# Kernel optimization log

Hardware: AMD Instinct MI355X
Metric: run time of the kernel (lower is better)

Reference implementation:

```python
import jax, jax.numpy as jnp
import numpy as np

STRIDE, K, PAD = 2, 4, 1
DN = ('NCH', 'OIH', 'NCH')


def conv1d(x, w, b):
    # w: (out, in, k); stride-2, pad-1 conv matching nn.Conv1d(k=4,s=2,p=1)
    y = jax.lax.conv_general_dilated(x, w, (STRIDE,), ((PAD, PAD),), dimension_numbers=DN)
    return y + b[None, :, None]


def conv_transpose1d(x, w, b):
    # w: (in, out, k) torch ConvTranspose1d layout. Equivalent forward conv:
    # dilate input by stride, pad k-1-p=2 each side, flipped+transposed kernel.
    wf = jnp.flip(w, -1).transpose(1, 0, 2)  # (out, in, k)
    y = jax.lax.conv_general_dilated(x, wf, (1,), ((K - 1 - PAD, K - 1 - PAD),),
                                     lhs_dilation=(STRIDE,), dimension_numbers=DN)
    return y + b[None, :, None]


def setup_inputs() -> dict:
    key = jax.random.key(0)
    ks = jax.random.split(key, 9)
    s = 0.1  # keep activations stable through 6 layers
    return {
        'x': jax.random.normal(ks[0], (16, 1, 65536), dtype=jnp.float32),
        'enc_w0': jax.random.normal(ks[1], (64, 1, 4), dtype=jnp.float32) * s,
        'enc_w': jax.random.normal(ks[2], (5, 64, 64, 4), dtype=jnp.float32) * s,
        'enc_b': jax.random.normal(ks[3], (6, 64), dtype=jnp.float32) * s,
        'codebook': jax.random.normal(ks[4], (1024, 64), dtype=jnp.float32),
        'dec_w': jax.random.normal(ks[5], (5, 64, 64, 4), dtype=jnp.float32) * s,
        'dec_w_last': jax.random.normal(ks[6], (64, 1, 4), dtype=jnp.float32) * s,
        'dec_b': jax.random.normal(ks[7], (5, 64), dtype=jnp.float32) * s,
        'dec_b_last': jax.random.normal(ks[8], (1,), dtype=jnp.float32) * s,
    }


def reference(x, enc_w0, enc_w, enc_b, codebook, dec_w, dec_w_last, dec_b, dec_b_last):
    B = x.shape[0]
    D = codebook.shape[1]

    h = jax.nn.relu(conv1d(x, enc_w0, enc_b[0]))
    for i in range(5):
        h = jax.nn.relu(conv1d(h, enc_w[i], enc_b[i + 1]))
    # h: (B, D, L'); flatten tokens
    z_e = h.transpose(0, 2, 1).reshape(-1, D)  # (B*L', D)

    # ---- Vector quantize: squared-distance argmin + gather ----
    dist = (jnp.sum(z_e * z_e, axis=1, keepdims=True)
            - 2.0 * z_e @ codebook.T
            + jnp.sum(codebook * codebook, axis=1)[None, :])  # (B*L', C)
    ids = jnp.argmin(dist, axis=-1)
    e = codebook[ids]
    e_k = z_e + jax.lax.stop_gradient(e - z_e)  # straight-through

    g = e_k.reshape(B, -1, D).transpose(0, 2, 1)  # (B, D, L')

    for i in range(5):
        g = jax.nn.relu(conv_transpose1d(g, dec_w[i], dec_b[i]))
    y = conv_transpose1d(g, dec_w_last, dec_b_last)
    return y, z_e, ids
```

## Files before the change

### kernel.cpp

```cpp
#include <hip/hip_runtime.h>

#define CH 64
#define TILE 128

typedef short s16x8 __attribute__((ext_vector_type(8)));
typedef float f32x4 __attribute__((ext_vector_type(4)));

static __device__ __forceinline__ ushort f2bf(float f) {
    union { float f; uint u; } v; v.f = f;
    const uint r = (v.u + 0x7FFFu + ((v.u >> 16) & 1u)) >> 16;
    return (ushort)r;
}
static __device__ __forceinline__ float bf2f(ushort u) {
    union { uint u; float f; } v; v.u = ((uint)u) << 16; return v.f;
}

__global__ __launch_bounds__(256) void k_prepack_enc(
    const float* __restrict__ enc_w, float* __restrict__ encW)
{
    const int idx = blockIdx.x * 256 + threadIdx.x;
    const int tau = idx & 3;
    const int o = (idx >> 2) & 63;
    const int i = (idx >> 8) & 63;
    const int L = idx >> 14;
    encW[idx] = enc_w[(((size_t)L * 64 + o) * 64 + i) * 4 + tau];
}

__device__ __forceinline__ void stage_half(
    const float* __restrict__ inb, float (*inT)[264], int half,
    int m0, int Lin, int tid)
{
    const int r = tid >> 3;
    const int i = half * 32 + r;
    const int seg = tid & 7;
    const float* src = inb + (size_t)i * Lin + 2 * m0 + 32 * seg;
    float* dst = inT[r] + 1 + 32 * seg;
#pragma unroll
    for (int t = 0; t < 8; ++t) {
        const float4 v = *(const float4*)(src + 4 * t);
        float* d = dst + 4 * t;
        d[0] = v.x;
        *(float2*)(d + 1) = make_float2(v.y, v.z);
        d[3] = v.w;
    }
    if (tid < 64) {
        const int rr = tid & 31, side = tid >> 5;
        const int pl = side ? 257 : 0;
        const int p = 2 * m0 - 1 + pl;
        inT[rr][pl] = (p >= 0 && p < Lin) ? inb[(size_t)(half * 32 + rr) * Lin + p] : 0.f;
    }
}

__device__ __forceinline__ void conv_accum_half(
    const float (*inT)[264], const float* __restrict__ wpk, int ibase,
    float acc[4][8], int og, int pg)
{
    const float* wI = wpk + og * 16 + (size_t)ibase * 256;
    for (int ii = 0; ii < 32; ++ii) {
        const float* wp = wI + ii * 256;
        const float4 w0 = *(const float4*)(wp + 0);
        const float4 w1 = *(const float4*)(wp + 4);
        const float4 w2 = *(const float4*)(wp + 8);
        const float4 w3 = *(const float4*)(wp + 12);
        const float* row = inT[ii];
#pragma unroll
        for (int j = 0; j < 4; ++j) {
            const int base = 4 * pg + 64 * j;
            const float2 xa = *(const float2*)(row + base);
            const float2 xb = *(const float2*)(row + base + 2);
            const float2 xc = *(const float2*)(row + base + 4);
            acc[0][2*j]   += w0.x * xa.x + w0.y * xa.y + w0.z * xb.x + w0.w * xb.y;
            acc[1][2*j]   += w1.x * xa.x + w1.y * xa.y + w1.z * xb.x + w1.w * xb.y;
            acc[2][2*j]   += w2.x * xa.x + w2.y * xa.y + w2.z * xb.x + w2.w * xb.y;
            acc[3][2*j]   += w3.x * xa.x + w3.y * xa.y + w3.z * xb.x + w3.w * xb.y;
            acc[0][2*j+1] += w0.x * xb.x + w0.y * xb.y + w0.z * xc.x + w0.w * xc.y;
            acc[1][2*j+1] += w1.x * xb.x + w1.y * xb.y + w1.z * xc.x + w1.w * xc.y;
            acc[2][2*j+1] += w2.x * xb.x + w2.y * xb.y + w2.z * xc.x + w2.w * xc.y;
            acc[3][2*j+1] += w3.x * xb.x + w3.y * xb.y + w3.z * xc.x + w3.w * xc.y;
        }
    }
}

__device__ __forceinline__ void conv_epilogue(
    float acc[4][8], float* __restrict__ out,
    int b, int m0, int Lout, int transpose, int og, int pg)
{
    if (!transpose) {
#pragma unroll
        for (int oo = 0; oo < 4; ++oo) {
            float* ob = out + ((size_t)b * CH + og * 4 + oo) * Lout + m0 + 2 * pg;
#pragma unroll
            for (int j = 0; j < 4; ++j) {
                float2 v;
                v.x = fmaxf(acc[oo][2*j], 0.f);
                v.y = fmaxf(acc[oo][2*j+1], 0.f);
                *(float2*)(ob + 32 * j) = v;
            }
        }
    } else {
#pragma unroll
        for (int j = 0; j < 4; ++j)
#pragma unroll
            for (int h = 0; h < 2; ++h) {
                const int ml = 2 * pg + 32 * j + h;
                float* ob = out + ((size_t)b * Lout + m0 + ml) * CH + og * 4;
                float4 v;
                v.x = fmaxf(acc[0][2*j+h], 0.f);
                v.y = fmaxf(acc[1][2*j+h], 0.f);
                v.z = fmaxf(acc[2][2*j+h], 0.f);
                v.w = fmaxf(acc[3][2*j+h], 0.f);
                *(float4*)ob = v;
            }
    }
}

__global__ __launch_bounds__(256) void k_enc_conv(
    const float* __restrict__ in, const float* __restrict__ wpk,
    const float* __restrict__ bias, float* __restrict__ out,
    int Lin, int Lout, int transpose)
{
    __shared__ float inT[32][264];
    const int m0 = blockIdx.x * TILE;
    const int b = blockIdx.y;
    const int tid = threadIdx.x;
    const int og = tid >> 4, pg = tid & 15;
    const float* inb = in + (size_t)b * CH * Lin;
    float acc[4][8];
#pragma unroll
    for (int oo = 0; oo < 4; ++oo) {
        const float bv = bias[og * 4 + oo];
#pragma unroll
        for (int j = 0; j < 8; ++j) acc[oo][j] = bv;
    }
    stage_half(inb, inT, 0, m0, Lin, tid);
    __syncthreads();
    conv_accum_half(inT, wpk, 0, acc, og, pg);
    __syncthreads();
    stage_half(inb, inT, 1, m0, Lin, tid);
    __syncthreads();
    conv_accum_half(inT, wpk, 32, acc, og, pg);
    conv_epilogue(acc, out, b, m0, Lout, transpose, og, pg);
}

__global__ __launch_bounds__(256) void k_enc01(
    const float* __restrict__ x, const float* __restrict__ w0,
    const float* __restrict__ b0, const float* __restrict__ wpk0,
    const float* __restrict__ b1, float* __restrict__ out)
{
    __shared__ float xl[520];
    __shared__ float e0s[32][264];
    const int m0 = blockIdx.x * TILE;
    const int b = blockIdx.y;
    const int tid = threadIdx.x;
    const int og = tid >> 4, pg = tid & 15;
    const float* xb = x + (size_t)b * 65536;
    const int x0i = 4 * m0 - 3;
    for (int xi = tid; xi < 518; xi += 256) {
        const int q = x0i + xi;
        xl[xi] = (q >= 0 && q < 65536) ? xb[q] : 0.f;
    }
    float acc[4][8];
#pragma unroll
    for (int oo = 0; oo < 4; ++oo) {
        const float bv = b1[og * 4 + oo];
#pragma unroll
        for (int j = 0; j < 8; ++j) acc[oo][j] = bv;
    }
    const int r = tid >> 3;
    const int oct = tid & 7;
    const int pbase = 2 * m0 - 1;
    __syncthreads();
    for (int half = 0; half < 2; ++half) {
        {
            const int i = half * 32 + r;
            const float4 wv = *(const float4*)(w0 + i * 4);
            const float bv = b0[i];
            for (int t = 0; t < 33; ++t) {
                const int pl = oct * 33 + t;
                if (pl < 258) {
                    const int pe = pbase + pl;
                    const float* xp = xl + 2 * pl;
                    const float v = wv.x * xp[0] + wv.y * xp[1] + wv.z * xp[2] + wv.w * xp[3] + bv;
                    e0s[r][pl] = (pe >= 0 && pe < 32768) ? fmaxf(v, 0.f) : 0.f;
                }
            }
        }
        __syncthreads();
        conv_accum_half(e0s, wpk0, half * 32, acc, og, pg);
        __syncthreads();
    }
    conv_epilogue(acc, out, b, m0, 16384, 0, og, pg);
}

__global__ __launch_bounds__(512) void k_vq(
    const float* __restrict__ z, const float* __restrict__ cb,
    float* __restrict__ idsf, float* __restrict__ g)
{
    __shared__ float c2s[1024];
    __shared__ float rval[8][64];
    __shared__ int   ridx[8][64];
    __shared__ int   widx[64];
    const int t0 = blockIdx.x * 64;
    const int tid = threadIdx.x;
    const int lane = tid & 63;
    const int wv = __builtin_amdgcn_readfirstlane(tid >> 6);

    for (int c = tid; c < 1024; c += 512) {
        const float* cp = cb + (size_t)c * 64;
        float s0 = 0.f, s1 = 0.f, s2 = 0.f, s3 = 0.f;
#pragma unroll
        for (int d = 0; d < 64; d += 4) {
            const float4 v = *(const float4*)(cp + d);
            s0 += v.x * v.x; s1 += v.y * v.y; s2 += v.z * v.z; s3 += v.w * v.w;
        }
        c2s[c] = (s0 + s1) + (s2 + s3);
    }
    float pz[64];
    {
        const float* zp = z + (size_t)(t0 + lane) * 64;
#pragma unroll
        for (int d = 0; d < 64; d += 4) {
            const float4 v = *(const float4*)(zp + d);
            pz[d] = -2.f * v.x; pz[d + 1] = -2.f * v.y;
            pz[d + 2] = -2.f * v.z; pz[d + 3] = -2.f * v.w;
        }
    }
    __syncthreads();
    float best = 3.0e38f; int bidx = 0;
    const int cbase = wv * 128;
    for (int cc = 0; cc < 128; ++cc) {
        const int code = cbase + cc;
        const float* cp = cb + (size_t)code * 64;
        float a0 = 0.f, a1 = 0.f, a2 = 0.f, a3 = 0.f;
#pragma unroll
        for (int d = 0; d < 64; d += 4) {
            a0 += cp[d] * pz[d];
            a1 += cp[d + 1] * pz[d + 1];
            a2 += cp[d + 2] * pz[d + 2];
            a3 += cp[d + 3] * pz[d + 3];
        }
        const float dist = c2s[code] + ((a0 + a1) + (a2 + a3));
        if (dist < best) { best = dist; bidx = code; }
    }
    rval[wv][lane] = best; ridx[wv][lane] = bidx;
    __syncthreads();
    if (tid < 64) {
        float bv = rval[0][tid]; int bi = ridx[0][tid];
#pragma unroll
        for (int k2 = 1; k2 < 8; ++k2) {
            const float v = rval[k2][tid];
            if (v < bv) { bv = v; bi = ridx[k2][tid]; }
        }
        widx[tid] = bi;
        idsf[t0 + tid] = (float)bi;
    }
    __syncthreads();
    const int bb = t0 >> 10;
    const int mb = t0 & 1023;
    for (int e = tid; e < 4096; e += 512) {
        const int tok = e & 63;
        const int d = e >> 6;
        g[((size_t)bb * CH + d) * 1024 + mb + tok] = cb[(size_t)widx[tok] * 64 + d];
    }
}

__global__ __launch_bounds__(256) void k_prepack(
    const float* __restrict__ dec_w, ushort* __restrict__ Afrag)
{
    const int idx = blockIdx.x * 256 + threadIdx.x;
    const int j    = idx & 7;
    const int lane = (idx >> 3) & 63;
    const int kt   = (idx >> 9) & 1;
    const int m    = (idx >> 10) & 3;
    const int tap  = (idx >> 12) & 3;
    const int L    = idx >> 14;
    const int o = m * 16 + (lane & 15);
    const int i = kt * 32 + ((lane >> 4) << 3) + j;
    Afrag[idx] = f2bf(dec_w[(((size_t)L * 64 + i) * 64 + o) * 4 + tap]);
}

__device__ __forceinline__ void stage_X(
    const float* __restrict__ Xb, ushort* __restrict__ Xs, int u0, int Lin, int tid)
{
    for (int e = tid; e < 272; e += 256) {
        const int i4 = (e & 15) * 4;
        const int u4 = e >> 4;
        const int bu = u0 - 2 + 4 * u4;
        float v[4][4];
        if (bu >= 0 && bu + 3 < Lin) {
            const float* src = Xb + (size_t)i4 * Lin + bu;
#pragma unroll
            for (int di = 0; di < 4; ++di) {
                const float4 t = *(const float4*)(src + (size_t)di * Lin);
                v[di][0] = t.x; v[di][1] = t.y; v[di][2] = t.z; v[di][3] = t.w;
            }
        } else {
#pragma unroll
            for (int di = 0; di < 4; ++di)
#pragma unroll
                for (int du = 0; du < 4; ++du) {
                    const int u = bu + du;
                    v[di][du] = (u >= 0 && u < Lin) ? Xb[(size_t)(i4 + di) * Lin + u] : 0.f;
                }
        }
#pragma unroll
        for (int du = 0; du < 4; ++du) {
            ushort4 pk;
            pk.x = f2bf(v[0][du]); pk.y = f2bf(v[1][du]);
            pk.z = f2bf(v[2][du]); pk.w = f2bf(v[3][du]);
            *(ushort4*)(Xs + (size_t)(4 * u4 + du) * 72 + i4) = pk;
        }
    }
}

__device__ __forceinline__ void dec_mfma_compute(
    const ushort* __restrict__ Xs, const ushort* __restrict__ AfragL,
    int tid, f32x4 accE[4], f32x4 accO[4], int& ul_out, int& kg_out, int& lane_out)
{
    const int lane = tid & 63;
    const int wave = tid >> 6;
    const int col = lane & 15, kg = lane >> 4;
    const int ul = wave * 16 + col;
    const ushort* basep = Xs + kg * 8;
    s16x8 Bm1[2], B0[2], Bp1[2];
#pragma unroll
    for (int kt = 0; kt < 2; ++kt) {
        Bm1[kt] = *(const s16x8*)(basep + (ul + 1) * 72 + kt * 32);
        B0[kt]  = *(const s16x8*)(basep + (ul + 2) * 72 + kt * 32);
        Bp1[kt] = *(const s16x8*)(basep + (ul + 3) * 72 + kt * 32);
    }
    const s16x8* Af = (const s16x8*)AfragL;
#pragma unroll
    for (int m = 0; m < 4; ++m) {
        f32x4 aE = {0.f, 0.f, 0.f, 0.f};
        f32x4 aO = {0.f, 0.f, 0.f, 0.f};
#pragma unroll
        for (int kt = 0; kt < 2; ++kt) {
            aE = __builtin_amdgcn_mfma_f32_16x16x32_bf16(
                Af[((1 * 4 + m) * 2 + kt) * 64 + lane], B0[kt], aE, 0, 0, 0);
            aE = __builtin_amdgcn_mfma_f32_16x16x32_bf16(
                Af[((3 * 4 + m) * 2 + kt) * 64 + lane], Bm1[kt], aE, 0, 0, 0);
            aO = __builtin_amdgcn_mfma_f32_16x16x32_bf16(
                Af[((2 * 4 + m) * 2 + kt) * 64 + lane], B0[kt], aO, 0, 0, 0);
            aO = __builtin_amdgcn_mfma_f32_16x16x32_bf16(
                Af[((0 * 4 + m) * 2 + kt) * 64 + lane], Bp1[kt], aO, 0, 0, 0);
        }
        accE[m] = aE;
        accO[m] = aO;
    }
    ul_out = ul; kg_out = kg; lane_out = lane;
}

__global__ __launch_bounds__(256) void k_dec2(
    const float* __restrict__ X, const ushort* __restrict__ AfragL,
    const float* __restrict__ bias, float* __restrict__ Y, int Lin)
{
    __shared__ ushort Xs[68 * 72];
    const int u0 = blockIdx.x * 64;
    const int b  = blockIdx.y;
    const int tid = threadIdx.x;
    const int Lout = Lin * 2;
    stage_X(X + (size_t)b * CH * Lin, Xs, u0, Lin, tid);
    __syncthreads();
    f32x4 accE[4], accO[4];
    int ul, kg, lane;
    dec_mfma_compute(Xs, AfragL, tid, accE, accO, ul, kg, lane);
    const int n2 = 2 * (u0 + ul);
#pragma unroll
    for (int m = 0; m < 4; ++m) {
        const float4 bm4 = *(const float4*)(bias + m * 16 + kg * 4);
        const float bb[4] = {bm4.x, bm4.y, bm4.z, bm4.w};
        float* yo = Y + ((size_t)b * CH + m * 16 + kg * 4) * Lout + n2;
#pragma unroll
        for (int r = 0; r < 4; ++r) {
            float2 v;
            v.x = fmaxf(accE[m][r] + bb[r], 0.f);
            v.y = fmaxf(accO[m][r] + bb[r], 0.f);
            *(float2*)(yo + (size_t)r * Lout) = v;
        }
    }
}

__global__ __launch_bounds__(256) void k_dec4y(
    const float* __restrict__ X, const ushort* __restrict__ AfragL,
    const float* __restrict__ w4, const float* __restrict__ bias,
    const float* __restrict__ wl, const float* __restrict__ blp,
    float* __restrict__ y)
{
    __shared__ ushort Xs[68 * 72];
    __shared__ float d4s[64][130];
    const int u0 = blockIdx.x * 64;
    const int b  = blockIdx.y;
    const int tid = threadIdx.x;
    const int Lin = 16384;
    stage_X(X + (size_t)b * CH * Lin, Xs, u0, Lin, tid);
    __syncthreads();
    f32x4 accE[4], accO[4];
    int ul, kg, lane;
    dec_mfma_compute(Xs, AfragL, tid, accE, accO, ul, kg, lane);
#pragma unroll
    for (int m = 0; m < 4; ++m) {
        const float4 bm4 = *(const float4*)(bias + m * 16 + kg * 4);
        const float bb[4] = {bm4.x, bm4.y, bm4.z, bm4.w};
#pragma unroll
        for (int r = 0; r < 4; ++r) {
            const int o = m * 16 + kg * 4 + r;
            d4s[o][2 * ul + 1] = fmaxf(accE[m][r] + bb[r], 0.f);
            d4s[o][2 * ul + 2] = fmaxf(accO[m][r] + bb[r], 0.f);
        }
    }
    {
        const int side = tid >> 7;
        const int o = (tid >> 1) & 63;
        const int half = tid & 1;
        const int ib = half * 32;
        float part = 0.f;
        if (side == 0) {
            for (int i = ib; i < ib + 32; ++i) {
                const float xu = bf2f(Xs[1 * 72 + i]);
                const float xp = bf2f(Xs[2 * 72 + i]);
                const float* wp = w4 + ((size_t)i * 64 + o) * 4;
                part += wp[2] * xu + wp[0] * xp;
            }
        } else {
            for (int i = ib; i < ib + 32; ++i) {
                const float xu = bf2f(Xs[66 * 72 + i]);
                const float xm = bf2f(Xs[65 * 72 + i]);
                const float* wp = w4 + ((size_t)i * 64 + o) * 4;
                part += wp[1] * xu + wp[3] * xm;
            }
        }
        part += __shfl_xor(part, 1);
        if (half == 0) {
            const float acc = bias[o] + part;
            if (side == 0) d4s[o][0]   = (u0 > 0)          ? fmaxf(acc, 0.f) : 0.f;
            else           d4s[o][129] = (u0 + 64 < 16384) ? fmaxf(acc, 0.f) : 0.f;
        }
    }
    __syncthreads();
    {
        const int odd = tid & 1;
        const int vl = (tid >> 1) + 1;
        float acc = blp[0];
        for (int o = 0; o < 64; ++o) {
            const float4 wv = *(const float4*)(wl + o * 4);
            const float xv = d4s[o][vl];
            const float xn = d4s[o][odd ? vl + 1 : vl - 1];
            acc += odd ? (wv.z * xv + wv.x * xn) : (wv.y * xv + wv.w * xn);
        }
        y[(size_t)b * 65536 + 4 * u0 + tid] = acc;
    }
}

extern "C" void kernel_launch(void* const* d_in, const int* in_sizes, int n_in,
                              void* d_out, int out_size, void* d_ws, size_t ws_size,
                              hipStream_t stream) {
    const float* x      = (const float*)d_in[0];
    const float* enc_w0 = (const float*)d_in[1];
    const float* enc_w  = (const float*)d_in[2];
    const float* enc_b  = (const float*)d_in[3];
    const float* cb     = (const float*)d_in[4];
    const float* dec_w  = (const float*)d_in[5];
    const float* dec_wl = (const float*)d_in[6];
    const float* dec_b  = (const float*)d_in[7];
    const float* dec_bl = (const float*)d_in[8];
    float* y    = (float*)d_out;
    float* z_e  = y + 1048576;
    float* idsf = y + 2097152;

    float* A  = (float*)d_ws;
    float* Bf = A + 16777216;

    float*  encW  = y + 14 * 65536;
    ushort* Afrag = (ushort*)(encW + 81920);

    k_prepack_enc<<<dim3(320), 256, 0, stream>>>(enc_w, encW);
    k_prepack<<<dim3(320), 256, 0, stream>>>(dec_w, Afrag);

    k_enc01<<<dim3(128, 16), 256, 0, stream>>>(x, enc_w0, enc_b, encW, enc_b + 64, A);
    k_enc_conv<<<dim3(64, 16), 256, 0, stream>>>(A,  encW + 1 * 16384, enc_b + 2 * 64, Bf, 16384, 8192, 0);
    k_enc_conv<<<dim3(32, 16), 256, 0, stream>>>(Bf, encW + 2 * 16384, enc_b + 3 * 64, A,  8192,  4096, 0);
    k_enc_conv<<<dim3(16, 16), 256, 0, stream>>>(A,  encW + 3 * 16384, enc_b + 4 * 64, Bf, 4096,  2048, 0);
    k_enc_conv<<<dim3(8, 16),  256, 0, stream>>>(Bf, encW + 4 * 16384, enc_b + 5 * 64, z_e, 2048, 1024, 1);
    k_vq<<<256, 512, 0, stream>>>(z_e, cb, idsf, A);

    k_dec2<<<dim3(16, 16),  256, 0, stream>>>(A,  Afrag + 0 * 16384, dec_b + 0 * 64, Bf, 1024);
    k_dec2<<<dim3(32, 16),  256, 0, stream>>>(Bf, Afrag + 1 * 16384, dec_b + 1 * 64, A,  2048);
    k_dec2<<<dim3(64, 16),  256, 0, stream>>>(A,  Afrag + 2 * 16384, dec_b + 2 * 64, Bf, 4096);
    k_dec2<<<dim3(128, 16), 256, 0, stream>>>(Bf, Afrag + 3 * 16384, dec_b + 3 * 64, A,  8192);
    (void)hipMemcpyAsync(Bf, Afrag + 4 * 16384, 16384 * sizeof(ushort),
                         hipMemcpyDeviceToDevice, stream);
    k_dec4y<<<dim3(256, 16), 256, 0, stream>>>(A, (const ushort*)Bf,
                                               dec_w + 4 * 16384, dec_b + 4 * 64,
                                               dec_wl, dec_bl, y);
}
```

Baseline: 542.6 us.

## Store decoder activations as padded channel-last bf16 and drop LDS staging

The VQ gather and every decoder layer now write their activations as bf16 in a token-major (length x 64 channels) layout, with one zero row of padding at each end of every batch. The MFMA B fragments are then loaded straight from global memory, so the per-block shared-memory staging, fp32-to-bf16 conversion and barrier are gone. This halves intermediate activation traffic and removes boundary checks. Small accumulator splits are also added to the final-layer scalar loops. The cost is that the padding rows must be zeroed correctly, and neighbouring blocks now re-read overlapping rows from global memory or cache.

```diff
diff --git a/kernel.cpp b/kernel.cpp
--- a/kernel.cpp
+++ b/kernel.cpp
@@ -194,7 +194,7 @@
 
 __global__ __launch_bounds__(512) void k_vq(
     const float* __restrict__ z, const float* __restrict__ cb,
-    float* __restrict__ idsf, float* __restrict__ g)
+    float* __restrict__ idsf, ushort* __restrict__ g)
 {
     __shared__ float c2s[1024];
     __shared__ float rval[8][64];
@@ -257,10 +257,19 @@
     __syncthreads();
     const int bb = t0 >> 10;
     const int mb = t0 & 1023;
+    ushort* gb = g + ((size_t)bb * 1026 + 1 + mb) * 64;
     for (int e = tid; e < 4096; e += 512) {
-        const int tok = e & 63;
-        const int d = e >> 6;
-        g[((size_t)bb * CH + d) * 1024 + mb + tok] = cb[(size_t)widx[tok] * 64 + d];
+        const int d = e & 63;
+        const int tok = e >> 6;
+        gb[(size_t)tok * 64 + d] = f2bf(cb[(size_t)widx[tok] * 64 + d]);
+    }
+    if (mb == 0 && tid < 16) {
+        ushort4 zz = {0, 0, 0, 0};
+        *(ushort4*)(g + ((size_t)bb * 1026) * 64 + tid * 4) = zz;
+    }
+    if (mb == 960 && tid < 16) {
+        ushort4 zz = {0, 0, 0, 0};
+        *(ushort4*)(g + ((size_t)bb * 1026 + 1025) * 64 + tid * 4) = zz;
     }
 }
 
@@ -279,55 +288,22 @@
     Afrag[idx] = f2bf(dec_w[(((size_t)L * 64 + i) * 64 + o) * 4 + tap]);
 }
 
-__device__ __forceinline__ void stage_X(
-    const float* __restrict__ Xb, ushort* __restrict__ Xs, int u0, int Lin, int tid)
-{
-    for (int e = tid; e < 272; e += 256) {
-        const int i4 = (e & 15) * 4;
-        const int u4 = e >> 4;
-        const int bu = u0 - 2 + 4 * u4;
-        float v[4][4];
-        if (bu >= 0 && bu + 3 < Lin) {
-            const float* src = Xb + (size_t)i4 * Lin + bu;
-#pragma unroll
-            for (int di = 0; di < 4; ++di) {
-                const float4 t = *(const float4*)(src + (size_t)di * Lin);
-                v[di][0] = t.x; v[di][1] = t.y; v[di][2] = t.z; v[di][3] = t.w;
-            }
-        } else {
-#pragma unroll
-            for (int di = 0; di < 4; ++di)
-#pragma unroll
-                for (int du = 0; du < 4; ++du) {
-                    const int u = bu + du;
-                    v[di][du] = (u >= 0 && u < Lin) ? Xb[(size_t)(i4 + di) * Lin + u] : 0.f;
-                }
-        }
-#pragma unroll
-        for (int du = 0; du < 4; ++du) {
-            ushort4 pk;
-            pk.x = f2bf(v[0][du]); pk.y = f2bf(v[1][du]);
-            pk.z = f2bf(v[2][du]); pk.w = f2bf(v[3][du]);
-            *(ushort4*)(Xs + (size_t)(4 * u4 + du) * 72 + i4) = pk;
-        }
-    }
-}
-
-__device__ __forceinline__ void dec_mfma_compute(
-    const ushort* __restrict__ Xs, const ushort* __restrict__ AfragL,
-    int tid, f32x4 accE[4], f32x4 accO[4], int& ul_out, int& kg_out, int& lane_out)
+__device__ __forceinline__ void dec_mfma_compute_g(
+    const ushort* __restrict__ Xb, const ushort* __restrict__ AfragL,
+    int u0, int tid, f32x4 accE[4], f32x4 accO[4],
+    int& ul_out, int& kg_out)
 {
     const int lane = tid & 63;
     const int wave = tid >> 6;
     const int col = lane & 15, kg = lane >> 4;
     const int ul = wave * 16 + col;
-    const ushort* basep = Xs + kg * 8;
+    const ushort* basep = Xb + (size_t)(u0 + ul) * 64 + kg * 8;
     s16x8 Bm1[2], B0[2], Bp1[2];
 #pragma unroll
     for (int kt = 0; kt < 2; ++kt) {
-        Bm1[kt] = *(const s16x8*)(basep + (ul + 1) * 72 + kt * 32);
-        B0[kt]  = *(const s16x8*)(basep + (ul + 2) * 72 + kt * 32);
-        Bp1[kt] = *(const s16x8*)(basep + (ul + 3) * 72 + kt * 32);
+        Bm1[kt] = *(const s16x8*)(basep - 64 + kt * 32);
+        B0[kt]  = *(const s16x8*)(basep + kt * 32);
+        Bp1[kt] = *(const s16x8*)(basep + 64 + kt * 32);
     }
     const s16x8* Af = (const s16x8*)AfragL;
 #pragma unroll
@@ -348,56 +324,66 @@
         accE[m] = aE;
         accO[m] = aO;
     }
-    ul_out = ul; kg_out = kg; lane_out = lane;
+    ul_out = ul; kg_out = kg;
 }
 
 __global__ __launch_bounds__(256) void k_dec2(
-    const float* __restrict__ X, const ushort* __restrict__ AfragL,
-    const float* __restrict__ bias, float* __restrict__ Y, int Lin)
-{
-    __shared__ ushort Xs[68 * 72];
+    const ushort* __restrict__ Xt, const ushort* __restrict__ AfragL,
+    const float* __restrict__ bias, ushort* __restrict__ Yt, int Lin)
+{
     const int u0 = blockIdx.x * 64;
     const int b  = blockIdx.y;
     const int tid = threadIdx.x;
     const int Lout = Lin * 2;
-    stage_X(X + (size_t)b * CH * Lin, Xs, u0, Lin, tid);
-    __syncthreads();
+    const ushort* Xb = Xt + ((size_t)b * (Lin + 2) + 1) * 64;
+    ushort* Yb = Yt + ((size_t)b * (Lout + 2) + 1) * 64;
+
     f32x4 accE[4], accO[4];
-    int ul, kg, lane;
-    dec_mfma_compute(Xs, AfragL, tid, accE, accO, ul, kg, lane);
-    const int n2 = 2 * (u0 + ul);
+    int ul, kg;
+    dec_mfma_compute_g(Xb, AfragL, u0, tid, accE, accO, ul, kg);
+    const size_t n2 = 2 * (size_t)(u0 + ul);
 #pragma unroll
     for (int m = 0; m < 4; ++m) {
         const float4 bm4 = *(const float4*)(bias + m * 16 + kg * 4);
         const float bb[4] = {bm4.x, bm4.y, bm4.z, bm4.w};
-        float* yo = Y + ((size_t)b * CH + m * 16 + kg * 4) * Lout + n2;
-#pragma unroll
-        for (int r = 0; r < 4; ++r) {
-            float2 v;
-            v.x = fmaxf(accE[m][r] + bb[r], 0.f);
-            v.y = fmaxf(accO[m][r] + bb[r], 0.f);
-            *(float2*)(yo + (size_t)r * Lout) = v;
-        }
+        ushort4 pe, po;
+        pe.x = f2bf(fmaxf(accE[m][0] + bb[0], 0.f));
+        pe.y = f2bf(fmaxf(accE[m][1] + bb[1], 0.f));
+        pe.z = f2bf(fmaxf(accE[m][2] + bb[2], 0.f));
+        pe.w = f2bf(fmaxf(accE[m][3] + bb[3], 0.f));
+        po.x = f2bf(fmaxf(accO[m][0] + bb[0], 0.f));
+        po.y = f2bf(fmaxf(accO[m][1] + bb[1], 0.f));
+        po.z = f2bf(fmaxf(accO[m][2] + bb[2], 0.f));
+        po.w = f2bf(fmaxf(accO[m][3] + bb[3], 0.f));
+        *(ushort4*)(Yb + n2 * 64 + m * 16 + kg * 4) = pe;
+        *(ushort4*)(Yb + (n2 + 1) * 64 + m * 16 + kg * 4) = po;
+    }
+    if (blockIdx.x == 0 && tid < 16) {
+        ushort4 zz = {0, 0, 0, 0};
+        *(ushort4*)(Yt + ((size_t)b * (Lout + 2)) * 64 + tid * 4) = zz;
+    }
+    if (u0 + 64 >= Lin && tid < 16) {
+        ushort4 zz = {0, 0, 0, 0};
+        *(ushort4*)(Yb + (size_t)Lout * 64 + tid * 4) = zz;
     }
 }
 
 __global__ __launch_bounds__(256) void k_dec4y(
-    const float* __restrict__ X, const ushort* __restrict__ AfragL,
+    const ushort* __restrict__ Xt, const ushort* __restrict__ AfragL,
     const float* __restrict__ w4, const float* __restrict__ bias,
     const float* __restrict__ wl, const float* __restrict__ blp,
     float* __restrict__ y)
 {
-    __shared__ ushort Xs[68 * 72];
     __shared__ float d4s[64][130];
     const int u0 = blockIdx.x * 64;
     const int b  = blockIdx.y;
     const int tid = threadIdx.x;
     const int Lin = 16384;
-    stage_X(X + (size_t)b * CH * Lin, Xs, u0, Lin, tid);
-    __syncthreads();
+    const ushort* Xb = Xt + ((size_t)b * (Lin + 2) + 1) * 64;
+
     f32x4 accE[4], accO[4];
-    int ul, kg, lane;
-    dec_mfma_compute(Xs, AfragL, tid, accE, accO, ul, kg, lane);
+    int ul, kg;
+    dec_mfma_compute_g(Xb, AfragL, u0, tid, accE, accO, ul, kg);
 #pragma unroll
     for (int m = 0; m < 4; ++m) {
         const float4 bm4 = *(const float4*)(bias + m * 16 + kg * 4);
@@ -414,22 +400,18 @@
         const int o = (tid >> 1) & 63;
         const int half = tid & 1;
         const int ib = half * 32;
-        float part = 0.f;
-        if (side == 0) {
-            for (int i = ib; i < ib + 32; ++i) {
-                const float xu = bf2f(Xs[1 * 72 + i]);
-                const float xp = bf2f(Xs[2 * 72 + i]);
-                const float* wp = w4 + ((size_t)i * 64 + o) * 4;
-                part += wp[2] * xu + wp[0] * xp;
-            }
-        } else {
-            for (int i = ib; i < ib + 32; ++i) {
-                const float xu = bf2f(Xs[66 * 72 + i]);
-                const float xm = bf2f(Xs[65 * 72 + i]);
-                const float* wp = w4 + ((size_t)i * 64 + o) * 4;
-                part += wp[1] * xu + wp[3] * xm;
-            }
-        }
+        float p0 = 0.f, p1 = 0.f;
+        const ushort* r0 = Xb + (size_t)(side ? (u0 + 64) : (u0 - 1)) * 64;
+        const ushort* r1 = Xb + (size_t)(side ? (u0 + 63) : u0) * 64;
+        const int tA = side ? 1 : 2;
+        const int tB = side ? 3 : 0;
+        for (int i = ib; i < ib + 32; i += 2) {
+            const float* wpa = w4 + ((size_t)i * 64 + o) * 4;
+            const float* wpb = w4 + ((size_t)(i + 1) * 64 + o) * 4;
+            p0 += wpa[tA] * bf2f(r0[i]) + wpa[tB] * bf2f(r1[i]);
+            p1 += wpb[tA] * bf2f(r0[i + 1]) + wpb[tB] * bf2f(r1[i + 1]);
+        }
+        float part = p0 + p1;
         part += __shfl_xor(part, 1);
         if (half == 0) {
             const float acc = bias[o] + part;
@@ -441,14 +423,22 @@
     {
         const int odd = tid & 1;
         const int vl = (tid >> 1) + 1;
-        float acc = blp[0];
-        for (int o = 0; o < 64; ++o) {
-            const float4 wv = *(const float4*)(wl + o * 4);
-            const float xv = d4s[o][vl];
-            const float xn = d4s[o][odd ? vl + 1 : vl - 1];
-            acc += odd ? (wv.z * xv + wv.x * xn) : (wv.y * xv + wv.w * xn);
-        }
-        y[(size_t)b * 65536 + 4 * u0 + tid] = acc;
+        float a0 = 0.f, a1 = 0.f, a2 = 0.f, a3 = 0.f;
+        for (int o = 0; o < 64; o += 4) {
+            const float4 w0 = *(const float4*)(wl + (o + 0) * 4);
+            const float4 w1 = *(const float4*)(wl + (o + 1) * 4);
+            const float4 w2 = *(const float4*)(wl + (o + 2) * 4);
+            const float4 w3 = *(const float4*)(wl + (o + 3) * 4);
+            const float xv0 = d4s[o + 0][vl], xn0 = d4s[o + 0][odd ? vl + 1 : vl - 1];
+            const float xv1 = d4s[o + 1][vl], xn1 = d4s[o + 1][odd ? vl + 1 : vl - 1];
+            const float xv2 = d4s[o + 2][vl], xn2 = d4s[o + 2][odd ? vl + 1 : vl - 1];
+            const float xv3 = d4s[o + 3][vl], xn3 = d4s[o + 3][odd ? vl + 1 : vl - 1];
+            a0 += odd ? (w0.z * xv0 + w0.x * xn0) : (w0.y * xv0 + w0.w * xn0);
+            a1 += odd ? (w1.z * xv1 + w1.x * xn1) : (w1.y * xv1 + w1.w * xn1);
+            a2 += odd ? (w2.z * xv2 + w2.x * xn2) : (w2.y * xv2 + w2.w * xn2);
+            a3 += odd ? (w3.z * xv3 + w3.x * xn3) : (w3.y * xv3 + w3.w * xn3);
+        }
+        y[(size_t)b * 65536 + 4 * u0 + tid] = blp[0] + ((a0 + a1) + (a2 + a3));
     }
 }
 
@@ -482,15 +472,15 @@
     k_enc_conv<<<dim3(32, 16), 256, 0, stream>>>(Bf, encW + 2 * 16384, enc_b + 3 * 64, A,  8192,  4096, 0);
     k_enc_conv<<<dim3(16, 16), 256, 0, stream>>>(A,  encW + 3 * 16384, enc_b + 4 * 64, Bf, 4096,  2048, 0);
     k_enc_conv<<<dim3(8, 16),  256, 0, stream>>>(Bf, encW + 4 * 16384, enc_b + 5 * 64, z_e, 2048, 1024, 1);
-    k_vq<<<256, 512, 0, stream>>>(z_e, cb, idsf, A);
-
-    k_dec2<<<dim3(16, 16),  256, 0, stream>>>(A,  Afrag + 0 * 16384, dec_b + 0 * 64, Bf, 1024);
-    k_dec2<<<dim3(32, 16),  256, 0, stream>>>(Bf, Afrag + 1 * 16384, dec_b + 1 * 64, A,  2048);
-    k_dec2<<<dim3(64, 16),  256, 0, stream>>>(A,  Afrag + 2 * 16384, dec_b + 2 * 64, Bf, 4096);
-    k_dec2<<<dim3(128, 16), 256, 0, stream>>>(Bf, Afrag + 3 * 16384, dec_b + 3 * 64, A,  8192);
+    k_vq<<<256, 512, 0, stream>>>(z_e, cb, idsf, (ushort*)A);
+
+    k_dec2<<<dim3(16, 16),  256, 0, stream>>>((const ushort*)A,  Afrag + 0 * 16384, dec_b + 0 * 64, (ushort*)Bf, 1024);
+    k_dec2<<<dim3(32, 16),  256, 0, stream>>>((const ushort*)Bf, Afrag + 1 * 16384, dec_b + 1 * 64, (ushort*)A,  2048);
+    k_dec2<<<dim3(64, 16),  256, 0, stream>>>((const ushort*)A,  Afrag + 2 * 16384, dec_b + 2 * 64, (ushort*)Bf, 4096);
+    k_dec2<<<dim3(128, 16), 256, 0, stream>>>((const ushort*)Bf, Afrag + 3 * 16384, dec_b + 3 * 64, (ushort*)A,  8192);
     (void)hipMemcpyAsync(Bf, Afrag + 4 * 16384, 16384 * sizeof(ushort),
                          hipMemcpyDeviceToDevice, stream);
-    k_dec4y<<<dim3(256, 16), 256, 0, stream>>>(A, (const ushort*)Bf,
+    k_dec4y<<<dim3(256, 16), 256, 0, stream>>>((const ushort*)A, (const ushort*)Bf,
                                                dec_w + 4 * 16384, dec_b + 4 * 64,
                                                dec_wl, dec_bl, y);
 }
```

Measured after the change: 533.7 us. Within noise of the previous version (-1.7%).
